# Performance work log

Hardware: AMD Instinct MI355X
Metric: run time of the kernel (lower is better)

The kernel has to match this reference:

```python
import jax, jax.numpy as jnp
import numpy as np

H = 8      # n_heads
DK = 64    # d_k per head
EPS = 1e-5       # InstanceNorm1d eps
SLOPE = 0.01     # LeakyReLU negative slope


def setup_inputs() -> dict:
    key = jax.random.key(0)
    ks = jax.random.split(key, 6)
    B, C, L = 16, 256, 1024
    HD = H * DK  # 512
    return {
        "x": jax.random.normal(ks[0], (B, C, L), dtype=jnp.float32),
        "Wq": jax.random.normal(ks[1], (HD, C), dtype=jnp.float32) * 0.02,
        "Wk": jax.random.normal(ks[2], (HD, C), dtype=jnp.float32) * 0.02,
        "Wv": jax.random.normal(ks[3], (HD, C), dtype=jnp.float32) * 0.02,
        "Wo": jax.random.normal(ks[4], (C, HD), dtype=jnp.float32) * 0.02,
        "gamma": jax.random.normal(ks[5], (1,), dtype=jnp.float32),
    }


def reference(x, Wq, Wk, Wv, Wo, gamma):
    B, C, L = x.shape
    # conv1x1 projections (bias=False) == channel matmuls -> [B, H*DK, L]
    # then reshape/permute into heads: [B, H, L, DK]
    def proj(W):
        y = jnp.einsum('oc,bcl->bol', W, x)          # [B, H*DK, L]
        return y.reshape(B, H, DK, L).transpose(0, 1, 3, 2)  # [B, H, L, DK]

    q, k, v = proj(Wq), proj(Wk), proj(Wv)
    # softmax-free linear attention: (Q K^T / d_k) V
    logits = jnp.einsum('bhld,bhmd->bhlm', q, k) / DK  # [B, H, L, L]
    out = jnp.einsum('bhlm,bhmd->bhld', logits, v)     # [B, H, L, DK]
    # merge heads back to channel-first [B, H*DK, L]
    merged = out.transpose(0, 1, 3, 2).reshape(B, H * DK, L)
    # output conv1x1 -> [B, C, L]
    o = jnp.einsum('oc,bcl->bol', Wo, merged)
    # InstanceNorm1d (affine=False): normalize over L per (b, c)
    mu = jnp.mean(o, axis=-1, keepdims=True)
    var = jnp.var(o, axis=-1, keepdims=True)
    o = (o - mu) * jax.lax.rsqrt(var + EPS)
    # gamma-scaled residual + LeakyReLU
    y = o * gamma + x
    return jnp.where(y >= 0, y, SLOPE * y)
```

## Files before the change

kernel.cpp:

```cpp
#include <hip/hip_runtime.h>

typedef __bf16 bf16;
typedef bf16 bf16x8 __attribute__((ext_vector_type(8)));
typedef bf16 bf16x4 __attribute__((ext_vector_type(4)));
typedef float f32x4 __attribute__((ext_vector_type(4)));

#define EPS 1e-5f
#define SLOPE 0.01f

__device__ __forceinline__ void gld_lds16(const bf16* g, bf16* l) {
    __builtin_amdgcn_global_load_lds(
        (const __attribute__((address_space(1))) unsigned int*)g,
        (__attribute__((address_space(3))) unsigned int*)l, 16, 0, 0);
}

__global__ __launch_bounds__(256) void prep_kernel(
    const float* __restrict__ x,
    const float* __restrict__ Wq, const float* __restrict__ Wk,
    const float* __restrict__ Wv, const float* __restrict__ Wo,
    bf16* __restrict__ xT, bf16* __restrict__ xB,
    bf16* __restrict__ WkvB, bf16* __restrict__ WqB, bf16* __restrict__ WoB)
{
    __shared__ float tile[64][65];
    const int id = blockIdx.x;
    const int t = threadIdx.x;
    if (id < 1024) {
        const int lt = id & 15, ct = (id >> 4) & 3, b = id >> 6;
        {
            const int cl = t >> 2;
            const int l4 = (t & 3) << 4;
            const float* src = x + (size_t)(b * 256 + ct * 64 + cl) * 1024 + lt * 64 + l4;
            float4 v0 = ((const float4*)src)[0];
            float4 v1 = ((const float4*)src)[1];
            float4 v2 = ((const float4*)src)[2];
            float4 v3 = ((const float4*)src)[3];
            bf16x8 r0, r1;
            r0[0]=(bf16)v0.x; r0[1]=(bf16)v0.y; r0[2]=(bf16)v0.z; r0[3]=(bf16)v0.w;
            r0[4]=(bf16)v1.x; r0[5]=(bf16)v1.y; r0[6]=(bf16)v1.z; r0[7]=(bf16)v1.w;
            r1[0]=(bf16)v2.x; r1[1]=(bf16)v2.y; r1[2]=(bf16)v2.z; r1[3]=(bf16)v2.w;
            r1[4]=(bf16)v3.x; r1[5]=(bf16)v3.y; r1[6]=(bf16)v3.z; r1[7]=(bf16)v3.w;
            bf16* xbd = xB + (size_t)(b * 256 + ct * 64 + cl) * 1024 + lt * 64 + l4;
            *(bf16x8*)xbd = r0;
            *(bf16x8*)(xbd + 8) = r1;
            float* tr = &tile[cl][l4];
            tr[0]=v0.x; tr[1]=v0.y; tr[2]=v0.z; tr[3]=v0.w;
            tr[4]=v1.x; tr[5]=v1.y; tr[6]=v1.z; tr[7]=v1.w;
            tr[8]=v2.x; tr[9]=v2.y; tr[10]=v2.z; tr[11]=v2.w;
            tr[12]=v3.x; tr[13]=v3.y; tr[14]=v3.z; tr[15]=v3.w;
        }
        __syncthreads();
        {
            const int lw = t >> 2;
            const int ec = (t & 3) << 4;
            bf16x8 o0, o1;
            #pragma unroll
            for (int ii = 0; ii < 8; ++ii) {
                o0[ii] = (bf16)tile[ec + ii][lw];
                o1[ii] = (bf16)tile[ec + 8 + ii][lw];
            }
            bf16* dst = xT + (size_t)(b * 1024 + lt * 64 + lw) * 256 + ct * 64 + ec;
            *(bf16x8*)dst = o0;
            *(bf16x8*)(dst + 8) = o1;
        }
    } else {
        const int i = (id - 1024) * 1024 + t * 4;
        const float* src; bf16* dst;
        if (i < 131072)      { src = Wk + i;            dst = WkvB + i; }
        else if (i < 262144) { src = Wv + (i - 131072); dst = WkvB + i; }
        else if (i < 393216) { src = Wq + (i - 262144); dst = WqB + (i - 262144); }
        else                 { src = Wo + (i - 393216); dst = WoB + (i - 393216); }
        float4 v = *(const float4*)src;
        bf16x4 o;
        o[0]=(bf16)v.x; o[1]=(bf16)v.y; o[2]=(bf16)v.z; o[3]=(bf16)v.w;
        *(bf16x4*)dst = o;
    }
}

__global__ __launch_bounds__(256) void qkv_gemm(
    const bf16* __restrict__ WkvB, const bf16* __restrict__ WqB,
    const bf16* __restrict__ xT, bf16* __restrict__ KV, bf16* __restrict__ Qt)
{
    __shared__ bf16 As[128 * 32];
    __shared__ bf16 Bs[128 * 32];
    int id = blockIdx.x;
    const bf16 *A, *Bt; bf16* C; int ldc, m0, n0;
    if (id < 1024) {
        const int z = id >> 6, rem = id & 63;
        m0 = (rem >> 3) * 128; n0 = (rem & 7) * 128;
        A = WkvB; Bt = xT + (size_t)z * 262144;
        C = KV + (size_t)z * 1048576; ldc = 1024;
    } else {
        id -= 1024;
        const int z = id >> 5, rem = id & 31;
        m0 = (rem >> 2) * 128; n0 = (rem & 3) * 128;
        A = xT + (size_t)z * 262144; Bt = WqB;
        C = Qt + (size_t)z * 524288; ldc = 512;
    }
    const int t = threadIdx.x, w = t >> 6, l = t & 63;
    const int srow = w * 16 + (l >> 2);
    const int ske  = (l & 3) * 8;
    const bf16* ga = A  + (size_t)(m0 + srow) * 256 + ske;
    const bf16* gb = Bt + (size_t)(n0 + srow) * 256 + ske;
    bf16* la = As + srow * 32 + ske;
    bf16* lb = Bs + srow * 32 + ske;
    const int lm = l & 15, lq = l >> 4;
    const int wm = (w & 1) * 64, wn = (w >> 1) * 64;

    f32x4 acc[4][4] = {};
    for (int kt = 0; kt < 8; ++kt) {
        const int k0 = kt * 32;
        gld_lds16(ga + k0, la);
        gld_lds16(ga + k0 + (size_t)64 * 256, la + 64 * 32);
        gld_lds16(gb + k0, lb);
        gld_lds16(gb + k0 + (size_t)64 * 256, lb + 64 * 32);
        __syncthreads();
        bf16x8 af[4], bfr[4];
        #pragma unroll
        for (int i = 0; i < 4; ++i)
            af[i] = *(const bf16x8*)(As + (wm + i * 16 + lm) * 32 + lq * 8);
        #pragma unroll
        for (int j = 0; j < 4; ++j)
            bfr[j] = *(const bf16x8*)(Bs + (wn + j * 16 + lm) * 32 + lq * 8);
        #pragma unroll
        for (int i = 0; i < 4; ++i)
            #pragma unroll
            for (int j = 0; j < 4; ++j)
                acc[i][j] = __builtin_amdgcn_mfma_f32_16x16x32_bf16(af[i], bfr[j], acc[i][j], 0, 0, 0);
        __syncthreads();
    }
    #pragma unroll
    for (int i = 0; i < 4; ++i)
        #pragma unroll
        for (int j = 0; j < 4; ++j) {
            const int row = m0 + wm + i * 16 + lq * 4;
            const int col = n0 + wn + j * 16 + lm;
            bf16* cp = C + (size_t)row * ldc + col;
            #pragma unroll
            for (int r = 0; r < 4; ++r)
                cp[(size_t)r * ldc] = (bf16)acc[i][j][r];
        }
}

template<int KDIM, typename OutT>
__global__ __launch_bounds__(256) void gemm128_bt(
    const bf16* __restrict__ A, const bf16* __restrict__ Bt, OutT* __restrict__ C,
    long long sBt, long long sC, int ldC)
{
    __shared__ bf16 As[128 * 32];
    __shared__ bf16 Bs[128 * 32];
    const int z = blockIdx.z;
    Bt += (size_t)z * sBt;
    C  += (size_t)z * sC;
    const int m0 = blockIdx.x * 128;
    const int n0 = blockIdx.y * 128;
    const int t = threadIdx.x, w = t >> 6, l = t & 63;
    const int srow = w * 16 + (l >> 2);
    const int ske  = (l & 3) * 8;
    const bf16* ga = A  + (size_t)(m0 + srow) * KDIM + ske;
    const bf16* gb = Bt + (size_t)(n0 + srow) * KDIM + ske;
    bf16* la = As + srow * 32 + ske;
    bf16* lb = Bs + srow * 32 + ske;
    const int lm = l & 15, lq = l >> 4;
    const int wm = (w & 1) * 64, wn = (w >> 1) * 64;

    f32x4 acc[4][4] = {};
    for (int kt = 0; kt < KDIM / 32; ++kt) {
        const int k0 = kt * 32;
        gld_lds16(ga + k0, la);
        gld_lds16(ga + k0 + (size_t)64 * KDIM, la + 64 * 32);
        gld_lds16(gb + k0, lb);
        gld_lds16(gb + k0 + (size_t)64 * KDIM, lb + 64 * 32);
        __syncthreads();
        bf16x8 af[4], bfr[4];
        #pragma unroll
        for (int i = 0; i < 4; ++i)
            af[i] = *(const bf16x8*)(As + (wm + i * 16 + lm) * 32 + lq * 8);
        #pragma unroll
        for (int j = 0; j < 4; ++j)
            bfr[j] = *(const bf16x8*)(Bs + (wn + j * 16 + lm) * 32 + lq * 8);
        #pragma unroll
        for (int i = 0; i < 4; ++i)
            #pragma unroll
            for (int j = 0; j < 4; ++j)
                acc[i][j] = __builtin_amdgcn_mfma_f32_16x16x32_bf16(af[i], bfr[j], acc[i][j], 0, 0, 0);
        __syncthreads();
    }
    #pragma unroll
    for (int i = 0; i < 4; ++i)
        #pragma unroll
        for (int j = 0; j < 4; ++j) {
            const int row = m0 + wm + i * 16 + lq * 4;
            const int col = n0 + wn + j * 16 + lm;
            OutT* cp = C + (size_t)row * ldC + col;
            #pragma unroll
            for (int r = 0; r < 4; ++r)
                cp[(size_t)r * ldC] = (OutT)acc[i][j][r];
        }
}

__global__ __launch_bounds__(256) void kvt_kernel(const bf16* __restrict__ KV,
                                                  bf16* __restrict__ T)
{
    __shared__ bf16 As[64 * 256];
    __shared__ bf16 Bs[64 * 256];
    const int bh = blockIdx.x;
    const int b = bh >> 3, h = bh & 7;
    const bf16* Kb = KV + (size_t)b * 1048576 + (size_t)(h * 64) * 1024;
    const bf16* Vb = KV + (size_t)b * 1048576 + (size_t)(512 + h * 64) * 1024;
    const int t = threadIdx.x, w = t >> 6, l = t & 63;
    const int lm = l & 15, lq = l >> 4;
    const int wm = (w & 1) * 32, wn = (w >> 1) * 32;
    const int lrow = l >> 5;
    const int lseg = l & 31;

    f32x4 acc[2][2] = {};
    for (int st = 0; st < 4; ++st) {
        const int k0 = st * 256;
        #pragma unroll
        for (int r = 0; r < 8; ++r) {
            const int row = w * 16 + r * 2 + lrow;
            const int gs = lseg ^ (row & 7);
            gld_lds16(Vb + (size_t)row * 1024 + k0 + gs * 8, As + row * 256 + lseg * 8);
            gld_lds16(Kb + (size_t)row * 1024 + k0 + gs * 8, Bs + row * 256 + lseg * 8);
        }
        __syncthreads();
        #pragma unroll
        for (int kc = 0; kc < 8; ++kc) {
            const int q = kc * 4 + lq;
            bf16x8 af[2], bfr[2];
            #pragma unroll
            for (int i = 0; i < 2; ++i) {
                const int m = wm + i * 16 + lm;
                af[i] = *(const bf16x8*)(As + m * 256 + (q ^ (m & 7)) * 8);
            }
            #pragma unroll
            for (int j = 0; j < 2; ++j) {
                const int n = wn + j * 16 + lm;
                bfr[j] = *(const bf16x8*)(Bs + n * 256 + (q ^ (n & 7)) * 8);
            }
            #pragma unroll
            for (int i = 0; i < 2; ++i)
                #pragma unroll
                for (int j = 0; j < 2; ++j)
                    acc[i][j] = __builtin_amdgcn_mfma_f32_16x16x32_bf16(af[i], bfr[j], acc[i][j], 0, 0, 0);
        }
        if (st < 3) __syncthreads();
    }
    #pragma unroll
    for (int i = 0; i < 2; ++i)
        #pragma unroll
        for (int j = 0; j < 2; ++j)
            #pragma unroll
            for (int r = 0; r < 4; ++r)
                T[(size_t)bh * 4096 + (size_t)(wm + i * 16 + lq * 4 + r) * 64 + wn + j * 16 + lm] =
                    (bf16)(acc[i][j][r] * 0.015625f);
}

__global__ __launch_bounds__(256) void gemm_merged(const bf16* __restrict__ Qt,
                                                   const bf16* __restrict__ T,
                                                   bf16* __restrict__ mT)
{
    __shared__ bf16 As[128 * 64];
    __shared__ bf16 Bs[64 * 64];
    const int mt = blockIdx.x;
    const int bh = blockIdx.y;
    const int b = bh >> 3, h = bh & 7;
    const int m0 = mt * 128;
    const int t = threadIdx.x, w = t >> 6, l = t & 63;
    const bf16* Ab = Qt + (size_t)b * 524288 + h * 64;
    const bf16* Bb = T  + (size_t)bh * 4096;
    const int lr = l >> 3;
    const int ls = l & 7;
    #pragma unroll
    for (int c = 0; c < 4; ++c) {
        const int row = c * 32 + w * 8 + lr;
        const int gs = ls ^ (row & 7);
        gld_lds16(Ab + (size_t)(m0 + row) * 512 + gs * 8, As + row * 64 + ls * 8);
    }
    #pragma unroll
    for (int c = 0; c < 2; ++c) {
        const int row = c * 32 + w * 8 + lr;
        const int gs = ls ^ (row & 7);
        gld_lds16(Bb + (size_t)row * 64 + gs * 8, Bs + row * 64 + ls * 8);
    }
    __syncthreads();
    const int lm = l & 15, lq = l >> 4;
    const int wm = w * 32;
    f32x4 acc[2][4] = {};
    #pragma unroll
    for (int ks = 0; ks < 2; ++ks) {
        const int q = ks * 4 + lq;
        bf16x8 af[2], bfr[4];
        #pragma unroll
        for (int i = 0; i < 2; ++i) {
            const int m = wm + i * 16 + lm;
            af[i] = *(const bf16x8*)(As + m * 64 + (q ^ (m & 7)) * 8);
        }
        #pragma unroll
        for (int j = 0; j < 4; ++j) {
            const int n = j * 16 + lm;
            bfr[j] = *(const bf16x8*)(Bs + n * 64 + (q ^ (n & 7)) * 8);
        }
        #pragma unroll
        for (int i = 0; i < 2; ++i)
            #pragma unroll
            for (int j = 0; j < 4; ++j)
                acc[i][j] = __builtin_amdgcn_mfma_f32_16x16x32_bf16(af[i], bfr[j], acc[i][j], 0, 0, 0);
    }
    #pragma unroll
    for (int i = 0; i < 2; ++i)
        #pragma unroll
        for (int j = 0; j < 4; ++j)
            #pragma unroll
            for (int r = 0; r < 4; ++r) {
                const int lrow = m0 + wm + i * 16 + lq * 4 + r;
                const int col  = h * 64 + j * 16 + lm;
                mT[(size_t)b * 524288 + (size_t)lrow * 512 + col] = (bf16)acc[i][j][r];
            }
}

__global__ __launch_bounds__(256) void norm_kernel(
    const bf16* __restrict__ o, const bf16* __restrict__ xB,
    const float* __restrict__ gamma, float* __restrict__ y)
{
    const size_t row = blockIdx.x;
    const bf16* orow = o + row * 1024;
    const bf16* xrow = xB + row * 1024;
    float* yrow = y + row * 1024;
    const int tid = threadIdx.x;

    bf16x4 ov = *(const bf16x4*)(orow + tid * 4);
    float4 v = {(float)ov[0], (float)ov[1], (float)ov[2], (float)ov[3]};
    float s  = v.x + v.y + v.z + v.w;
    float ss = v.x * v.x + v.y * v.y + v.z * v.z + v.w * v.w;
    #pragma unroll
    for (int off = 32; off > 0; off >>= 1) {
        s  += __shfl_down(s, off);
        ss += __shfl_down(ss, off);
    }
    __shared__ float red[10];
    const int wave = tid >> 6, lane = tid & 63;
    if (lane == 0) { red[wave] = s; red[4 + wave] = ss; }
    __syncthreads();
    if (tid == 0) {
        float a  = red[0] + red[1] + red[2] + red[3];
        float b2 = red[4] + red[5] + red[6] + red[7];
        float mu = a * (1.0f / 1024.0f);
        float var = b2 * (1.0f / 1024.0f) - mu * mu;
        red[8] = mu;
        red[9] = rsqrtf(var + EPS);
    }
    __syncthreads();
    const float mu = red[8], inv = red[9], g = gamma[0];
    bf16x4 xv4 = *(const bf16x4*)(xrow + tid * 4);
    float4 r;
    r.x = (v.x - mu) * inv * g + (float)xv4[0];
    r.y = (v.y - mu) * inv * g + (float)xv4[1];
    r.z = (v.z - mu) * inv * g + (float)xv4[2];
    r.w = (v.w - mu) * inv * g + (float)xv4[3];
    r.x = r.x >= 0.f ? r.x : SLOPE * r.x;
    r.y = r.y >= 0.f ? r.y : SLOPE * r.y;
    r.z = r.z >= 0.f ? r.z : SLOPE * r.z;
    r.w = r.w >= 0.f ? r.w : SLOPE * r.w;
    ((float4*)yrow)[tid] = r;
}

extern "C" void kernel_launch(void* const* d_in, const int* in_sizes, int n_in,
                              void* d_out, int out_size, void* d_ws, size_t ws_size,
                              hipStream_t stream) {
    const float* x     = (const float*)d_in[0];
    const float* Wq    = (const float*)d_in[1];
    const float* Wk    = (const float*)d_in[2];
    const float* Wv    = (const float*)d_in[3];
    const float* Wo    = (const float*)d_in[4];
    const float* gamma = (const float*)d_in[5];
    float* y = (float*)d_out;

    char* wsb = (char*)d_ws;
    bf16* xT   = (bf16*)(wsb);
    bf16* xB   = (bf16*)(wsb +  8388608);
    bf16* WkvB = (bf16*)(wsb + 16777216);
    bf16* WqB  = (bf16*)(wsb + 17301504);
    bf16* WoB  = (bf16*)(wsb + 17563648);
    bf16* KV   = (bf16*)(wsb + 17825792);
    bf16* Qt   = (bf16*)(wsb + 51380224);
    bf16* T    = (bf16*)(wsb + 68157440);
    bf16* mT   = (bf16*)(wsb + 69206016);
    bf16* o    = (bf16*)(wsb + 85983232);

    prep_kernel<<<dim3(1536), 256, 0, stream>>>(x, Wq, Wk, Wv, Wo, xT, xB, WkvB, WqB, WoB);
    qkv_gemm<<<dim3(1536), 256, 0, stream>>>(WkvB, WqB, xT, KV, Qt);
    kvt_kernel<<<dim3(128), 256, 0, stream>>>(KV, T);
    gemm_merged<<<dim3(8, 128), 256, 0, stream>>>(Qt, T, mT);
    gemm128_bt<512, bf16><<<dim3(2, 8, 16), 256, 0, stream>>>(WoB, mT, o, 524288LL, 262144LL, 1024);
    norm_kernel<<<dim3(4096), 256, 0, stream>>>(o, xB, gamma, y);
}
```

Before: 139.4 us.

## Reassociate linear attention through the input Gram matrix to shrink GEMMs

Because the attention has no softmax, the whole chain is linear in x. The output is rewritten as Wo·(Wq^T·(Wk·G·Wv^T)/64)·x with G = x·x^T per batch. Instead of projecting Q, K and V over the full sequence, it computes the 256x256 Gram matrix, small weight-space products per head, a combined per-batch 256x256 weight, and one final GEMM over L. This cuts the large intermediate KV/Qt tensors and their memory traffic. In exchange it adds more small, low-occupancy launches and changes the bf16 rounding points, for example G is rounded to bf16 after a K=1024 reduction.

```diff
diff --git a/kernel.cpp b/kernel.cpp
--- a/kernel.cpp
+++ b/kernel.cpp
@@ -19,7 +19,8 @@
     const float* __restrict__ Wq, const float* __restrict__ Wk,
     const float* __restrict__ Wv, const float* __restrict__ Wo,
     bf16* __restrict__ xT, bf16* __restrict__ xB,
-    bf16* __restrict__ WkvB, bf16* __restrict__ WqB, bf16* __restrict__ WoB)
+    bf16* __restrict__ WkB, bf16* __restrict__ WvB,
+    bf16* __restrict__ WoB, bf16* __restrict__ WqT)
 {
     __shared__ float tile[64][65];
     const int id = blockIdx.x;
@@ -62,93 +63,59 @@
             *(bf16x8*)dst = o0;
             *(bf16x8*)(dst + 8) = o1;
         }
-    } else {
+    } else if (id < 1408) {
         const int i = (id - 1024) * 1024 + t * 4;
         const float* src; bf16* dst;
-        if (i < 131072)      { src = Wk + i;            dst = WkvB + i; }
-        else if (i < 262144) { src = Wv + (i - 131072); dst = WkvB + i; }
-        else if (i < 393216) { src = Wq + (i - 262144); dst = WqB + (i - 262144); }
-        else                 { src = Wo + (i - 393216); dst = WoB + (i - 393216); }
+        if (i < 131072)      { src = Wk + i;            dst = WkB + i; }
+        else if (i < 262144) { src = Wv + (i - 131072); dst = WvB + (i - 131072); }
+        else                 { src = Wo + (i - 262144); dst = WoB + (i - 262144); }
         float4 v = *(const float4*)src;
         bf16x4 o;
         o[0]=(bf16)v.x; o[1]=(bf16)v.y; o[2]=(bf16)v.z; o[3]=(bf16)v.w;
         *(bf16x4*)dst = o;
-    }
-}
-
-__global__ __launch_bounds__(256) void qkv_gemm(
-    const bf16* __restrict__ WkvB, const bf16* __restrict__ WqB,
-    const bf16* __restrict__ xT, bf16* __restrict__ KV, bf16* __restrict__ Qt)
-{
-    __shared__ bf16 As[128 * 32];
-    __shared__ bf16 Bs[128 * 32];
-    int id = blockIdx.x;
-    const bf16 *A, *Bt; bf16* C; int ldc, m0, n0;
-    if (id < 1024) {
-        const int z = id >> 6, rem = id & 63;
-        m0 = (rem >> 3) * 128; n0 = (rem & 7) * 128;
-        A = WkvB; Bt = xT + (size_t)z * 262144;
-        C = KV + (size_t)z * 1048576; ldc = 1024;
     } else {
-        id -= 1024;
-        const int z = id >> 5, rem = id & 31;
-        m0 = (rem >> 2) * 128; n0 = (rem & 3) * 128;
-        A = xT + (size_t)z * 262144; Bt = WqB;
-        C = Qt + (size_t)z * 524288; ldc = 512;
-    }
-    const int t = threadIdx.x, w = t >> 6, l = t & 63;
-    const int srow = w * 16 + (l >> 2);
-    const int ske  = (l & 3) * 8;
-    const bf16* ga = A  + (size_t)(m0 + srow) * 256 + ske;
-    const bf16* gb = Bt + (size_t)(n0 + srow) * 256 + ske;
-    bf16* la = As + srow * 32 + ske;
-    bf16* lb = Bs + srow * 32 + ske;
-    const int lm = l & 15, lq = l >> 4;
-    const int wm = (w & 1) * 64, wn = (w >> 1) * 64;
-
-    f32x4 acc[4][4] = {};
-    for (int kt = 0; kt < 8; ++kt) {
-        const int k0 = kt * 32;
-        gld_lds16(ga + k0, la);
-        gld_lds16(ga + k0 + (size_t)64 * 256, la + 64 * 32);
-        gld_lds16(gb + k0, lb);
-        gld_lds16(gb + k0 + (size_t)64 * 256, lb + 64 * 32);
-        __syncthreads();
-        bf16x8 af[4], bfr[4];
-        #pragma unroll
-        for (int i = 0; i < 4; ++i)
-            af[i] = *(const bf16x8*)(As + (wm + i * 16 + lm) * 32 + lq * 8);
-        #pragma unroll
-        for (int j = 0; j < 4; ++j)
-            bfr[j] = *(const bf16x8*)(Bs + (wn + j * 16 + lm) * 32 + lq * 8);
-        #pragma unroll
-        for (int i = 0; i < 4; ++i)
-            #pragma unroll
-            for (int j = 0; j < 4; ++j)
-                acc[i][j] = __builtin_amdgcn_mfma_f32_16x16x32_bf16(af[i], bfr[j], acc[i][j], 0, 0, 0);
-        __syncthreads();
-    }
-    #pragma unroll
-    for (int i = 0; i < 4; ++i)
-        #pragma unroll
-        for (int j = 0; j < 4; ++j) {
-            const int row = m0 + wm + i * 16 + lq * 4;
-            const int col = n0 + wn + j * 16 + lm;
-            bf16* cp = C + (size_t)row * ldc + col;
-            #pragma unroll
-            for (int r = 0; r < 4; ++r)
-                cp[(size_t)r * ldc] = (bf16)acc[i][j][r];
-        }
+        const int id2 = id - 1408;
+        const int h = id2 >> 2, ct = id2 & 3;
+        {
+            const int e  = t >> 2;
+            const int c4 = (t & 3) << 4;
+            const float* src = Wq + (size_t)(h * 64 + e) * 256 + ct * 64 + c4;
+            float4 v0 = ((const float4*)src)[0];
+            float4 v1 = ((const float4*)src)[1];
+            float4 v2 = ((const float4*)src)[2];
+            float4 v3 = ((const float4*)src)[3];
+            float* tr = &tile[e][c4];
+            tr[0]=v0.x; tr[1]=v0.y; tr[2]=v0.z; tr[3]=v0.w;
+            tr[4]=v1.x; tr[5]=v1.y; tr[6]=v1.z; tr[7]=v1.w;
+            tr[8]=v2.x; tr[9]=v2.y; tr[10]=v2.z; tr[11]=v2.w;
+            tr[12]=v3.x; tr[13]=v3.y; tr[14]=v3.z; tr[15]=v3.w;
+        }
+        __syncthreads();
+        {
+            const int c  = t >> 2;
+            const int e4 = (t & 3) << 4;
+            bf16x8 o0, o1;
+            #pragma unroll
+            for (int ii = 0; ii < 8; ++ii) {
+                o0[ii] = (bf16)tile[e4 + ii][c];
+                o1[ii] = (bf16)tile[e4 + 8 + ii][c];
+            }
+            bf16* dst = WqT + (size_t)h * 16384 + (size_t)(ct * 64 + c) * 64 + e4;
+            *(bf16x8*)dst = o0;
+            *(bf16x8*)(dst + 8) = o1;
+        }
+    }
 }
 
 template<int KDIM, typename OutT>
 __global__ __launch_bounds__(256) void gemm128_bt(
     const bf16* __restrict__ A, const bf16* __restrict__ Bt, OutT* __restrict__ C,
-    long long sBt, long long sC, int ldC)
+    long long sA, long long sBt, long long sC, int ldC)
 {
     __shared__ bf16 As[128 * 32];
     __shared__ bf16 Bs[128 * 32];
     const int z = blockIdx.z;
+    A  += (size_t)z * sA;
     Bt += (size_t)z * sBt;
     C  += (size_t)z * sC;
     const int m0 = blockIdx.x * 128;
@@ -198,124 +165,97 @@
         }
 }
 
-__global__ __launch_bounds__(256) void kvt_kernel(const bf16* __restrict__ KV,
-                                                  bf16* __restrict__ T)
+__global__ __launch_bounds__(256) void tm_kernel(
+    const bf16* __restrict__ S, const bf16* __restrict__ WkB,
+    const bf16* __restrict__ WqT, bf16* __restrict__ WmT)
 {
-    __shared__ bf16 As[64 * 256];
-    __shared__ bf16 Bs[64 * 256];
+    __shared__ __align__(16) bf16 regA[16384];
+    __shared__ __align__(16) bf16 Qb[16384];
+    bf16* Sc = regA;
+    bf16* Kc = regA + 8192;
+    bf16* Tb = regA;
+
     const int bh = blockIdx.x;
     const int b = bh >> 3, h = bh & 7;
-    const bf16* Kb = KV + (size_t)b * 1048576 + (size_t)(h * 64) * 1024;
-    const bf16* Vb = KV + (size_t)b * 1048576 + (size_t)(512 + h * 64) * 1024;
+    const bf16* Sg = S   + (size_t)b * 131072 + (size_t)h * 64 * 256;
+    const bf16* Kg = WkB + (size_t)h * 64 * 256;
+    const bf16* Qg = WqT + (size_t)h * 16384;
     const int t = threadIdx.x, w = t >> 6, l = t & 63;
     const int lm = l & 15, lq = l >> 4;
-    const int wm = (w & 1) * 32, wn = (w >> 1) * 32;
-    const int lrow = l >> 5;
-    const int lseg = l & 31;
-
-    f32x4 acc[2][2] = {};
-    for (int st = 0; st < 4; ++st) {
-        const int k0 = st * 256;
-        #pragma unroll
-        for (int r = 0; r < 8; ++r) {
-            const int row = w * 16 + r * 2 + lrow;
-            const int gs = lseg ^ (row & 7);
-            gld_lds16(Vb + (size_t)row * 1024 + k0 + gs * 8, As + row * 256 + lseg * 8);
-            gld_lds16(Kb + (size_t)row * 1024 + k0 + gs * 8, Bs + row * 256 + lseg * 8);
-        }
-        __syncthreads();
-        #pragma unroll
-        for (int kc = 0; kc < 8; ++kc) {
-            const int q = kc * 4 + lq;
-            bf16x8 af[2], bfr[2];
-            #pragma unroll
-            for (int i = 0; i < 2; ++i) {
-                const int m = wm + i * 16 + lm;
-                af[i] = *(const bf16x8*)(As + m * 256 + (q ^ (m & 7)) * 8);
+
+    #pragma unroll
+    for (int it = 0; it < 8; ++it) {
+        const int idx = it * 256 + t;
+        const int r = idx >> 3, s = idx & 7;
+        gld_lds16(Qg + (size_t)r * 64 + (s ^ (r & 7)) * 8, Qb + r * 64 + s * 8);
+    }
+
+    f32x4 accT[4] = {};
+    for (int ck = 0; ck < 2; ++ck) {
+        const int k0 = ck * 128;
+        #pragma unroll
+        for (int it = 0; it < 4; ++it) {
+            const int idx = it * 256 + t;
+            const int r = idx >> 4, s = idx & 15;
+            const int gs = (s ^ (r & 7)) * 8;
+            gld_lds16(Sg + (size_t)r * 256 + k0 + gs, Sc + r * 128 + s * 8);
+            gld_lds16(Kg + (size_t)r * 256 + k0 + gs, Kc + r * 128 + s * 8);
+        }
+        __syncthreads();
+        #pragma unroll
+        for (int ks = 0; ks < 4; ++ks) {
+            const int q = ks * 4 + lq;
+            const int ra = w * 16 + lm;
+            bf16x8 a = *(const bf16x8*)(Sc + ra * 128 + (q ^ (ra & 7)) * 8);
+            #pragma unroll
+            for (int nf = 0; nf < 4; ++nf) {
+                const int rb = nf * 16 + lm;
+                bf16x8 bb = *(const bf16x8*)(Kc + rb * 128 + (q ^ (rb & 7)) * 8);
+                accT[nf] = __builtin_amdgcn_mfma_f32_16x16x32_bf16(a, bb, accT[nf], 0, 0, 0);
             }
-            #pragma unroll
-            for (int j = 0; j < 2; ++j) {
-                const int n = wn + j * 16 + lm;
-                bfr[j] = *(const bf16x8*)(Bs + n * 256 + (q ^ (n & 7)) * 8);
-            }
-            #pragma unroll
-            for (int i = 0; i < 2; ++i)
-                #pragma unroll
-                for (int j = 0; j < 2; ++j)
-                    acc[i][j] = __builtin_amdgcn_mfma_f32_16x16x32_bf16(af[i], bfr[j], acc[i][j], 0, 0, 0);
-        }
-        if (st < 3) __syncthreads();
-    }
-    #pragma unroll
-    for (int i = 0; i < 2; ++i)
-        #pragma unroll
-        for (int j = 0; j < 2; ++j)
-            #pragma unroll
-            for (int r = 0; r < 4; ++r)
-                T[(size_t)bh * 4096 + (size_t)(wm + i * 16 + lq * 4 + r) * 64 + wn + j * 16 + lm] =
-                    (bf16)(acc[i][j][r] * 0.015625f);
-}
-
-__global__ __launch_bounds__(256) void gemm_merged(const bf16* __restrict__ Qt,
-                                                   const bf16* __restrict__ T,
-                                                   bf16* __restrict__ mT)
-{
-    __shared__ bf16 As[128 * 64];
-    __shared__ bf16 Bs[64 * 64];
-    const int mt = blockIdx.x;
-    const int bh = blockIdx.y;
-    const int b = bh >> 3, h = bh & 7;
-    const int m0 = mt * 128;
-    const int t = threadIdx.x, w = t >> 6, l = t & 63;
-    const bf16* Ab = Qt + (size_t)b * 524288 + h * 64;
-    const bf16* Bb = T  + (size_t)bh * 4096;
-    const int lr = l >> 3;
-    const int ls = l & 7;
-    #pragma unroll
-    for (int c = 0; c < 4; ++c) {
-        const int row = c * 32 + w * 8 + lr;
-        const int gs = ls ^ (row & 7);
-        gld_lds16(Ab + (size_t)(m0 + row) * 512 + gs * 8, As + row * 64 + ls * 8);
-    }
-    #pragma unroll
-    for (int c = 0; c < 2; ++c) {
-        const int row = c * 32 + w * 8 + lr;
-        const int gs = ls ^ (row & 7);
-        gld_lds16(Bb + (size_t)row * 64 + gs * 8, Bs + row * 64 + ls * 8);
-    }
+        }
+        __syncthreads();
+    }
+    #pragma unroll
+    for (int nf = 0; nf < 4; ++nf)
+        #pragma unroll
+        for (int ri = 0; ri < 4; ++ri) {
+            const int row = w * 16 + lq * 4 + ri;
+            const int col = nf * 16 + lm;
+            Tb[row * 64 + (((col >> 3) ^ (row & 7)) << 3) + (col & 7)] =
+                (bf16)(accT[nf][ri] * 0.015625f);
+        }
     __syncthreads();
-    const int lm = l & 15, lq = l >> 4;
-    const int wm = w * 32;
-    f32x4 acc[2][4] = {};
+
+    f32x4 accM[4][4] = {};
     #pragma unroll
     for (int ks = 0; ks < 2; ++ks) {
         const int q = ks * 4 + lq;
-        bf16x8 af[2], bfr[4];
-        #pragma unroll
-        for (int i = 0; i < 2; ++i) {
-            const int m = wm + i * 16 + lm;
-            af[i] = *(const bf16x8*)(As + m * 64 + (q ^ (m & 7)) * 8);
-        }
-        #pragma unroll
-        for (int j = 0; j < 4; ++j) {
-            const int n = j * 16 + lm;
-            bfr[j] = *(const bf16x8*)(Bs + n * 64 + (q ^ (n & 7)) * 8);
-        }
-        #pragma unroll
-        for (int i = 0; i < 2; ++i)
-            #pragma unroll
-            for (int j = 0; j < 4; ++j)
-                acc[i][j] = __builtin_amdgcn_mfma_f32_16x16x32_bf16(af[i], bfr[j], acc[i][j], 0, 0, 0);
-    }
-    #pragma unroll
-    for (int i = 0; i < 2; ++i)
-        #pragma unroll
-        for (int j = 0; j < 4; ++j)
-            #pragma unroll
-            for (int r = 0; r < 4; ++r) {
-                const int lrow = m0 + wm + i * 16 + lq * 4 + r;
-                const int col  = h * 64 + j * 16 + lm;
-                mT[(size_t)b * 524288 + (size_t)lrow * 512 + col] = (bf16)acc[i][j][r];
+        bf16x8 bfrag[4];
+        #pragma unroll
+        for (int nf = 0; nf < 4; ++nf) {
+            const int rb = nf * 16 + lm;
+            bfrag[nf] = *(const bf16x8*)(Tb + rb * 64 + (q ^ (rb & 7)) * 8);
+        }
+        #pragma unroll
+        for (int mf = 0; mf < 4; ++mf) {
+            const int ra = w * 64 + mf * 16 + lm;
+            bf16x8 a = *(const bf16x8*)(Qb + ra * 64 + (q ^ (ra & 7)) * 8);
+            #pragma unroll
+            for (int nf = 0; nf < 4; ++nf)
+                accM[mf][nf] = __builtin_amdgcn_mfma_f32_16x16x32_bf16(a, bfrag[nf], accM[mf][nf], 0, 0, 0);
+        }
+    }
+    bf16* Wg = WmT + (size_t)b * 131072 + h * 64;
+    #pragma unroll
+    for (int mf = 0; mf < 4; ++mf)
+        #pragma unroll
+        for (int nf = 0; nf < 4; ++nf)
+            #pragma unroll
+            for (int ri = 0; ri < 4; ++ri) {
+                const int c = w * 64 + mf * 16 + lq * 4 + ri;
+                const int d = nf * 16 + lm;
+                Wg[(size_t)c * 512 + d] = (bf16)accM[mf][nf][ri];
             }
 }
 
@@ -377,21 +317,33 @@
     float* y = (float*)d_out;
 
     char* wsb = (char*)d_ws;
-    bf16* xT   = (bf16*)(wsb);
-    bf16* xB   = (bf16*)(wsb +  8388608);
-    bf16* WkvB = (bf16*)(wsb + 16777216);
-    bf16* WqB  = (bf16*)(wsb + 17301504);
-    bf16* WoB  = (bf16*)(wsb + 17563648);
-    bf16* KV   = (bf16*)(wsb + 17825792);
-    bf16* Qt   = (bf16*)(wsb + 51380224);
-    bf16* T    = (bf16*)(wsb + 68157440);
-    bf16* mT   = (bf16*)(wsb + 69206016);
-    bf16* o    = (bf16*)(wsb + 85983232);
-
-    prep_kernel<<<dim3(1536), 256, 0, stream>>>(x, Wq, Wk, Wv, Wo, xT, xB, WkvB, WqB, WoB);
-    qkv_gemm<<<dim3(1536), 256, 0, stream>>>(WkvB, WqB, xT, KV, Qt);
-    kvt_kernel<<<dim3(128), 256, 0, stream>>>(KV, T);
-    gemm_merged<<<dim3(8, 128), 256, 0, stream>>>(Qt, T, mT);
-    gemm128_bt<512, bf16><<<dim3(2, 8, 16), 256, 0, stream>>>(WoB, mT, o, 524288LL, 262144LL, 1024);
+    bf16* xT  = (bf16*)(wsb);
+    bf16* xB  = (bf16*)(wsb +  8388608);
+    bf16* WkB = (bf16*)(wsb + 16777216);
+    bf16* WvB = (bf16*)(wsb + 17039360);
+    bf16* WoB = (bf16*)(wsb + 17301504);
+    bf16* WqT = (bf16*)(wsb + 17563648);
+    bf16* G   = (bf16*)(wsb + 17825792);
+    bf16* S   = (bf16*)(wsb + 19922944);
+    bf16* WmT = (bf16*)(wsb + 24117248);
+    bf16* Wt  = (bf16*)(wsb + 28311552);
+    bf16* o   = (bf16*)(wsb + 30408704);
+
+    prep_kernel<<<dim3(1440), 256, 0, stream>>>(x, Wq, Wk, Wv, Wo, xT, xB, WkB, WvB, WoB, WqT);
+
+    gemm128_bt<1024, bf16><<<dim3(2, 2, 16), 256, 0, stream>>>(
+        xB, xB, G, 262144LL, 262144LL, 65536LL, 256);
+
+    gemm128_bt<256, bf16><<<dim3(4, 2, 16), 256, 0, stream>>>(
+        WvB, G, S, 0LL, 65536LL, 131072LL, 256);
+
+    tm_kernel<<<dim3(128), 256, 0, stream>>>(S, WkB, WqT, WmT);
+
+    gemm128_bt<512, bf16><<<dim3(2, 2, 16), 256, 0, stream>>>(
+        WoB, WmT, Wt, 0LL, 131072LL, 65536LL, 256);
+
+    gemm128_bt<256, bf16><<<dim3(2, 8, 16), 256, 0, stream>>>(
+        Wt, xT, o, 65536LL, 262144LL, 262144LL, 1024);
+
     norm_kernel<<<dim3(4096), 256, 0, stream>>>(o, xB, gamma, y);
 }
```

Result: no change. 139.0 us (-0.3%).
